# Kernel optimization log

Measured on AMD Instinct MI355X. Metric: run time of the kernel, lower is better.

Reference implementation:

```python
import jax, jax.numpy as jnp
import numpy as np

D = 64
NU = 30000
NI = 20000
LU = 50  # mailbox length at user nodes (item_max_length)
LI = 50  # mailbox length at item nodes (user_max_length)


def setup_inputs() -> dict:
    key = jax.random.key(0)
    ks = jax.random.split(key, 14)
    s = 0.05
    return {
        "user_feat": jax.random.normal(ks[0], (NU, D), jnp.float32),
        "item_feat": jax.random.normal(ks[1], (NI, D), jnp.float32),
        "W_u": jax.random.normal(ks[2], (D, D), jnp.float32) * s,
        "W_i": jax.random.normal(ks[3], (D, D), jnp.float32) * s,
        "Wg_u": jax.random.normal(ks[4], (2 * D, D), jnp.float32) * s,
        "Wg_i": jax.random.normal(ks[5], (2 * D, D), jnp.float32) * s,
        "i_te": jax.random.normal(ks[6], (LI, D), jnp.float32) * s,
        "i_te_k": jax.random.normal(ks[7], (LI, D), jnp.float32) * s,
        "u_te": jax.random.normal(ks[8], (LU, D), jnp.float32) * s,
        "u_te_k": jax.random.normal(ks[9], (LU, D), jnp.float32) * s,
        "item_nbr": jax.random.randint(ks[10], (NI, LI), 0, NU, jnp.int32),
        "item_time": jax.random.randint(ks[11], (NI, LI), 0, 1000000, jnp.int32),
        "user_nbr": jax.random.randint(ks[12], (NU, LU), 0, NI, jnp.int32),
        "user_time": jax.random.randint(ks[13], (NU, LU), 0, 1000000, jnp.int32),
    }


def _orgat_att(src_mb, dst_h, time, te, te_k):
    """One DGSR reduce: long-term time-encoded attention + short-term last-attention.
    src_mb: [N, L, d] gathered source features; dst_h: [N, d]; time: [N, L] int.
    Returns concat([h_long, h_short]) @ Wg applied by caller.
    """
    L = time.shape[1]
    d = src_mb.shape[-1]
    scale = jnp.sqrt(jnp.asarray(d, src_mb.dtype))
    # rank of each edge's time within the neighborhood; re_order: 0 = most recent
    rank = jnp.argsort(jnp.argsort(time, axis=1), axis=1)
    re_o = L - rank - 1                                       # [N, L]
    e = jnp.sum((te[re_o] + src_mb) * dst_h[:, None, :], axis=2) / scale
    alpha = jax.nn.softmax(e, axis=1)                         # [N, L]
    h_long = jnp.sum(alpha[..., None] * (src_mb + te_k[re_o]), axis=1)
    # short-term: attention keyed on the most-recent neighbor
    last = jnp.argmax(time, axis=1)
    last_em = jnp.take_along_axis(src_mb, last[:, None, None], axis=1)  # [N,1,d]
    e1 = jnp.sum(last_em * src_mb, axis=2) / scale
    a1 = jax.nn.softmax(e1, axis=1)
    h_short = jnp.sum(a1[..., None] * src_mb, axis=1)
    return jnp.concatenate([h_long, h_short], axis=-1)        # [N, 2d]


def reference(user_feat, item_feat, W_u, W_i, Wg_u, Wg_i, i_te, i_te_k,
              u_te, u_te_k, item_nbr, item_time, user_nbr, user_time):
    uh = user_feat @ W_u   # user_weight (feat_drop=0)
    ih = item_feat @ W_i   # item_weight
    # 'by' edges: users -> items (item reduce uses user mailboxes + i_time_encoding)
    u_mb = uh[item_nbr]                                        # [NI, LI, d]
    item_new = _orgat_att(u_mb, ih, item_time, i_te, i_te_k) @ Wg_i
    # 'pby' edges: items -> users (user reduce uses item mailboxes + u_time_encoding)
    i_mb = ih[user_nbr]                                        # [NU, LU, d]
    user_new = _orgat_att(i_mb, uh, user_time, u_te, u_te_k) @ Wg_u
    # residual update functions
    user_out = jax.nn.elu(user_new + user_feat)
    item_out = jax.nn.elu(item_new + item_feat)
    return user_out, item_out
```

## Files before the change

### kernel.cpp

```cpp
#include <hip/hip_runtime.h>
#include <stdint.h>

#define D   64
#define L   50
#define NUM_U 30000
#define NUM_I 20000
#define MROWS 50
#define PW3 (MROWS * 32 + 96 + 192)
#define GEMM_BLKS 782


typedef __attribute__((ext_vector_type(8))) short short8x;
typedef __attribute__((ext_vector_type(4))) float f32x4;

__device__ __forceinline__ float lof(unsigned int u) {
    union { unsigned int i; float f; } v; v.i = u << 16; return v.f;
}
__device__ __forceinline__ float hif(unsigned int u) {
    union { unsigned int i; float f; } v; v.i = u & 0xffff0000u; return v.f;
}
__device__ __forceinline__ unsigned int f2bfbits(float f) {
    union { float f; unsigned int i; } v; v.f = f;
    return (v.i + 0x7fffu + ((v.i >> 16) & 1u)) >> 16;
}
__device__ __forceinline__ unsigned int packbf(float a, float b) {
    return f2bfbits(a) | (f2bfbits(b) << 16);
}
__device__ __forceinline__ float rl(float v, int l) {
    return __int_as_float(__builtin_amdgcn_readlane(__float_as_int(v), l));
}
__device__ __forceinline__ int rli(int v, int l) {
    return __builtin_amdgcn_readlane(v, l);
}
__device__ __forceinline__ void gload_lds16(const void* g, void* l) {
    __builtin_amdgcn_global_load_lds(
        (const __attribute__((address_space(1))) unsigned int*)g,
        (__attribute__((address_space(3))) unsigned int*)l, 16, 0, 0);
}

__global__ __launch_bounds__(256) void prep(
    const float* __restrict__ user_feat, const float* __restrict__ item_feat,
    const float* __restrict__ W_u, const float* __restrict__ W_i,
    const float* __restrict__ Wg_i, const float* __restrict__ Wg_u,
    const float* __restrict__ te_i, const float* __restrict__ te_u,
    const float* __restrict__ tk_i, const float* __restrict__ tk_u,
    unsigned int* __restrict__ H,
    unsigned short* __restrict__ WgPi, unsigned short* __restrict__ WgPu,
    unsigned short* __restrict__ tePi, unsigned short* __restrict__ tePu,
    unsigned short* __restrict__ tkPi, unsigned short* __restrict__ tkPu)
{
    const int tid = threadIdx.x;
    if (blockIdx.x < GEMM_BLKS) {
        const int lane = tid & 63, wid = tid >> 6;
        const int tile = blockIdx.x * 4 + wid;
        if (tile >= 3125) return;
        const int r0 = tile * 16;
        const float* src; const float* W;
        if (r0 < NUM_U) { src = user_feat + (size_t)r0 * D;            W = W_u; }
        else            { src = item_feat + (size_t)(r0 - NUM_U) * D;  W = W_i; }
        const int q4 = lane >> 4, c16 = lane & 15;

        short8x bf[2];
#pragma unroll
        for (int kt = 0; kt < 2; kt++) {
            const float* fp = src + c16 * D + kt * 32 + q4 * 8;
            float4 x = *(const float4*)fp;
            float4 y = *(const float4*)(fp + 4);
            union { short8x v; unsigned int u[4]; } t2;
            t2.u[0] = packbf(x.x, x.y); t2.u[1] = packbf(x.z, x.w);
            t2.u[2] = packbf(y.x, y.y); t2.u[3] = packbf(y.z, y.w);
            bf[kt] = t2.v;
        }
        f32x4 zero4 = {0.f, 0.f, 0.f, 0.f};
        f32x4 acc[4];
#pragma unroll
        for (int mt = 0; mt < 4; mt++) acc[mt] = zero4;
#pragma unroll
        for (int kt = 0; kt < 2; kt++) {
#pragma unroll
            for (int mt = 0; mt < 4; mt++) {
                union { short8x v; unsigned short u[8]; } a;
#pragma unroll
                for (int j = 0; j < 8; j++)
                    a.u[j] = (unsigned short)f2bfbits(
                        W[(kt * 32 + q4 * 8 + j) * D + c16 + 16 * mt]);
                acc[mt] = __builtin_amdgcn_mfma_f32_16x16x32_bf16(a.v, bf[kt], acc[mt], 0, 0, 0);
            }
        }
        unsigned int* Hrow = H + (size_t)(r0 + c16) * 32;
#pragma unroll
        for (int mt = 0; mt < 4; mt++) {
            uint2 pk;
            pk.x = packbf(acc[mt][0], acc[mt][1]);
            pk.y = packbf(acc[mt][2], acc[mt][3]);
            *(uint2*)(Hrow + 8 * mt + 2 * q4) = pk;
        }
    } else {
        int gid = (blockIdx.x - GEMM_BLKS) * 256 + tid;
        for (int idx = gid; idx < 8192; idx += 4096) {
            int n = idx >> 7, k = idx & 127;
            WgPi[idx] = (unsigned short)f2bfbits(Wg_i[k * 64 + n]);
            WgPu[idx] = (unsigned short)f2bfbits(Wg_u[k * 64 + n]);
        }
        {
            int idx = gid;
            int r = idx >> 6, k = idx & 63;
            tePi[idx] = (r < L) ? (unsigned short)f2bfbits(te_i[r * 64 + k]) : 0;
            tePu[idx] = (r < L) ? (unsigned short)f2bfbits(te_u[r * 64 + k]) : 0;
            int d = idx >> 6, rr = idx & 63;
            tkPi[idx] = (rr < L) ? (unsigned short)f2bfbits(tk_i[rr * 64 + d]) : 0;
            tkPu[idx] = (rr < L) ? (unsigned short)f2bfbits(tk_u[rr * 64 + d]) : 0;
        }
    }
}

__global__ __launch_bounds__(256, 5) void attn_fused(
    const unsigned int* __restrict__ H,
    const float* __restrict__ user_feat, const float* __restrict__ item_feat,
    const unsigned short* __restrict__ WgPi, const unsigned short* __restrict__ WgPu,
    const unsigned short* __restrict__ tePi, const unsigned short* __restrict__ tePu,
    const unsigned short* __restrict__ tkPi, const unsigned short* __restrict__ tkPu,
    const int* __restrict__ item_nbr, const int* __restrict__ item_time,
    const int* __restrict__ user_nbr, const int* __restrict__ user_time,
    float* __restrict__ out)
{
    __shared__ unsigned int lds[4 * PW3];

    const int tid = threadIdx.x, lane = tid & 63, wid = tid >> 6;
    const bool iside = blockIdx.x < (NUM_I / 4);
    const int bb = iside ? blockIdx.x : blockIdx.x - NUM_I / 4;
    const int n = bb * 4 + wid;
    const int src_base = iside ? 0 : NUM_U;
    const int dst_base = iside ? NUM_U : 0;
    const float* dst_feat = iside ? item_feat : user_feat;
    const unsigned short* WgP  = iside ? WgPi : WgPu;
    const unsigned short* teP  = iside ? tePi : tePu;
    const unsigned short* tekP = iside ? tkPi : tkPu;
    const int* nbr   = iside ? item_nbr  : user_nbr;
    const int* timev = iside ? item_time : user_time;
    float* outp = out + (iside ? (size_t)NUM_U * D : 0);

    const int q4 = lane >> 4, c16 = lane & 15;

    const unsigned int*   Hsrc = H + (size_t)src_base * 32;
    const unsigned short* Hs16 = (const unsigned short*)H + (size_t)src_base * 64;
    const unsigned short* Hd16 = (const unsigned short*)H + (size_t)dst_base * 64;

    unsigned int*   wld  = lds + wid * PW3;
    unsigned int*   mbw  = wld;
    unsigned short* dla  = (unsigned short*)(wld + MROWS * 32);
    float*          escf = (float*)(wld + MROWS * 32 + 96);
    unsigned short* cat  = (unsigned short*)(wld + MROWS * 32 + 96);

    int t   = (lane < L) ? timev[(size_t)n * L + lane] : 0;
    int nbv = (lane < L) ? nbr[(size_t)n * L + lane]  : 0;

    {
        const int soff = (((lane & 7) ^ (lane >> 3)) << 4);
        const int rsel = (lane >> 3) << 2;
#pragma unroll
        for (int g = 0; g < 6; g++) {
            int nb = __builtin_amdgcn_ds_bpermute(rsel + (g << 5), nbv);
            const char* gp = (const char*)(Hsrc + (size_t)(unsigned)nb * 32) + soff;
            gload_lds16(gp, (char*)mbw + (g << 10));
        }
        int row = 48 + (lane >> 5), d = lane & 31;
        int nb = __builtin_amdgcn_ds_bpermute(row << 2, nbv);
        unsigned int v = Hsrc[(size_t)(unsigned)nb * 32 + d];
        mbw[(row << 5) + ((((d >> 2) ^ (row & 7)) << 2) | (d & 3))] = v;
    }

    unsigned int key  = (lane < L) ? ((((unsigned)t) << 6) | (unsigned)lane) : 0u;
    unsigned int key2 = (lane < L) ? ((((unsigned)t) << 6) | (unsigned)(63 - lane)) : 0u;
    int rank = 0;
#pragma unroll
    for (int j = 0; j < L; j++) {
        unsigned int kj = (unsigned int)rli((int)key, j);
        rank += (kj < key) ? 1 : 0;
    }
    int re_o = (lane < L) ? (L - 1 - rank) : lane;

    unsigned int m2 = key2;
#pragma unroll
    for (int s = 32; s; s >>= 1) { unsigned int o2 = __shfl_xor(m2, s); m2 = (o2 > m2) ? o2 : m2; }
    const int last = 63 - (int)(m2 & 63u);

    dla[lane] = Hd16[(size_t)n * 64 + lane];
    int nbl = __shfl(nbv, last);
    dla[64 + lane] = Hs16[(size_t)(unsigned)nbl * 64 + lane];

    f32x4 zero4 = {0.f, 0.f, 0.f, 0.f};
    f32x4 acc_e[4], acc_t[4];
#pragma unroll
    for (int nt = 0; nt < 4; nt++) { acc_e[nt] = zero4; acc_t[nt] = zero4; }
    __builtin_amdgcn_s_setprio(1);
#pragma unroll
    for (int kt = 0; kt < 2; kt++) {
        short8x afr = *(const short8x*)(dla + (c16 & 1) * 64 + kt * 32 + q4 * 8);
        int cc = kt * 4 + q4;
#pragma unroll
        for (int nt = 0; nt < 4; nt++) {
            int row = c16 + 16 * nt;
            int rowc = (row < MROWS) ? row : 0;
            short8x bv = *(const short8x*)((const char*)mbw + rowc * 128
                                           + ((cc ^ (rowc & 7)) << 4));
            acc_e[nt] = __builtin_amdgcn_mfma_f32_16x16x32_bf16(afr, bv, acc_e[nt], 0, 0, 0);
            short8x bt = *(const short8x*)(teP + row * 64 + kt * 32 + q4 * 8);
            acc_t[nt] = __builtin_amdgcn_mfma_f32_16x16x32_bf16(afr, bt, acc_t[nt], 0, 0, 0);
        }
    }
    __builtin_amdgcn_s_setprio(0);
    if (q4 == 0) {
#pragma unroll
        for (int nt = 0; nt < 4; nt++) {
            escf[c16 + 16 * nt]       = acc_e[nt][0];
            escf[64 + c16 + 16 * nt]  = acc_e[nt][1];
            escf[128 + c16 + 16 * nt] = acc_t[nt][0];
        }
    }
    float e  = escf[lane];
    float e1 = escf[64 + lane];
    float th = escf[128 + re_o];

    e = (e + th) * 0.125f;
    e1 *= 0.125f;
    if (lane >= L) { e = -3e38f; e1 = -3e38f; }

    float mx = e;
#pragma unroll
    for (int s = 32; s; s >>= 1) { float o2 = __shfl_xor(mx, s); mx = (o2 > mx) ? o2 : mx; }
    float ex = __expf(e - mx);
    float sm = ex;
#pragma unroll
    for (int s = 32; s; s >>= 1) sm += __shfl_xor(sm, s);
    float alpha = ex / sm;

    float mx1 = e1;
#pragma unroll
    for (int s = 32; s; s >>= 1) { float o2 = __shfl_xor(mx1, s); mx1 = (o2 > mx1) ? o2 : mx1; }
    float ex1 = __expf(e1 - mx1);
    float sm1 = ex1;
#pragma unroll
    for (int s = 32; s; s >>= 1) sm1 += __shfl_xor(sm1, s);
    float aw = ex1 / sm1;

    dla[lane]       = (unsigned short)f2bfbits(alpha);
    dla[64 + lane]  = (unsigned short)f2bfbits(aw);
    dla[128 + re_o] = (unsigned short)f2bfbits(alpha);

    f32x4 acc_s[4], acc_k[4];
#pragma unroll
    for (int nt = 0; nt < 4; nt++) { acc_s[nt] = zero4; acc_k[nt] = zero4; }
    __builtin_amdgcn_s_setprio(1);
#pragma unroll
    for (int kt = 0; kt < 2; kt++) {
        short8x aS = *(const short8x*)(dla + (c16 & 1) * 64 + kt * 32 + q4 * 8);
        short8x aB = *(const short8x*)(dla + 128 + kt * 32 + q4 * 8);
        int kr128[8];
#pragma unroll
        for (int i = 0; i < 8; i++) {
            int k = kt * 32 + q4 * 8 + i;
            if (kt) k = (k < MROWS) ? k : (k - 32);
            kr128[i] = k << 7;
        }
#pragma unroll
        for (int nt = 0; nt < 4; nt++) {
            int dc = c16 + 16 * nt;
            int t3 = dc >> 3;
            const char* cbase = (const char*)mbw + ((dc & 7) << 1);
            union { short8x v; unsigned short u[8]; } bu;
#pragma unroll
            for (int i = 0; i < 8; i++)
                bu.u[i] = *(const unsigned short*)(cbase + kr128[i] + ((t3 ^ i) << 4));
            acc_s[nt] = __builtin_amdgcn_mfma_f32_16x16x32_bf16(aS, bu.v, acc_s[nt], 0, 0, 0);
            short8x bK = *(const short8x*)(tekP + dc * 64 + kt * 32 + q4 * 8);
            acc_k[nt] = __builtin_amdgcn_mfma_f32_16x16x32_bf16(aB, bK, acc_k[nt], 0, 0, 0);
        }
    }
    __builtin_amdgcn_s_setprio(0);
    if (q4 == 0) {
#pragma unroll
        for (int nt = 0; nt < 4; nt++) {
            cat[c16 + 16 * nt]      = (unsigned short)f2bfbits(acc_s[nt][0] + acc_k[nt][0]);
            cat[64 + c16 + 16 * nt] = (unsigned short)f2bfbits(acc_s[nt][1]);
        }
    }
    __syncthreads();

    short8x bfr[4];
#pragma unroll
    for (int tK = 0; tK < 4; tK++)
        bfr[tK] = *(const short8x*)(WgP + (wid * 16 + c16) * 128 + tK * 32 + q4 * 8);

    const unsigned short* catw =
        (const unsigned short*)(lds + (lane & 3) * PW3 + MROWS * 32 + 96);
    f32x4 acc = zero4;
#pragma unroll
    for (int tK = 0; tK < 4; tK++) {
        short8x a = *(const short8x*)(catw + tK * 32 + q4 * 8);
        acc = __builtin_amdgcn_mfma_f32_16x16x32_bf16(a, bfr[tK], acc, 0, 0, 0);
    }
    float r01 = (q4 & 1) ? acc[1] : acc[0];
    float r23 = (q4 & 1) ? acc[3] : acc[2];
    float pv  = (q4 & 2) ? r23 : r01;

    int node = bb * 4 + q4;
    float fres = dst_feat[(size_t)node * D + wid * 16 + c16];
    float oo = pv + fres;
    oo = (oo > 0.f) ? oo : (__expf(oo) - 1.f);
    outp[(size_t)node * D + wid * 16 + c16] = oo;
}

__global__ __launch_bounds__(256) void attn_mono(
    const float* __restrict__ src_feat, const float* __restrict__ dst_feat,
    const float* __restrict__ W_src, const float* __restrict__ W_dst,
    const float* __restrict__ Wg, const float* __restrict__ te,
    const float* __restrict__ tek, const int* __restrict__ nbr,
    const int* __restrict__ timev, float* __restrict__ out)
{
    __shared__ unsigned int ws32[64 * 33];
    __shared__ unsigned int te32[L * 33];
    __shared__ unsigned int mbs[4][L * 33];
    const int tid = threadIdx.x, lane = tid & 63, wid = tid >> 6;
    const int n = blockIdx.x * 4 + wid;
    {
        const float2* Wf2 = (const float2*)W_src;
        const float2* Te2 = (const float2*)te;
        for (int idx = tid; idx < 2048; idx += 256) {
            float2 w = Wf2[idx];
            ws32[(idx >> 5) * 33 + (idx & 31)] = packbf(w.x, w.y);
            if (idx < 1600) {
                float2 t2 = Te2[idx];
                te32[(idx >> 5) * 33 + (idx & 31)] = packbf(t2.x, t2.y);
            }
        }
    }
    __syncthreads();
    int t  = (lane < L) ? timev[(size_t)n * L + lane] : 0;
    int nb = (lane < L) ? nbr[(size_t)n * L + lane]  : 0;
    unsigned int key  = (lane < L) ? ((((unsigned)t) << 6) | (unsigned)lane) : 0u;
    unsigned int key2 = (lane < L) ? ((((unsigned)t) << 6) | (unsigned)(63 - lane)) : 0u;
    int rank = 0;
#pragma unroll
    for (int j = 0; j < L; j++) {
        unsigned int kj = (unsigned int)rli((int)key, j);
        rank += (kj < key) ? 1 : 0;
    }
    int re_o = (lane < L) ? (L - 1 - rank) : 0;
    unsigned int m2 = key2;
#pragma unroll
    for (int s = 32; s; s >>= 1) { unsigned int o2 = __shfl_xor(m2, s); m2 = (o2 > m2) ? o2 : m2; }
    const int last = 63 - (int)(m2 & 63u);
    const int rr = (lane < L) ? lane : (L - 1);
    float f = dst_feat[(size_t)n * D + lane];
    float dh;
    {
        float b0 = 0.f, b1 = 0.f, b2 = 0.f, b3 = 0.f;
#pragma unroll
        for (int k = 0; k < 64; k += 4) {
            b0 += rl(f, k + 0) * W_dst[(k + 0) * 64 + lane];
            b1 += rl(f, k + 1) * W_dst[(k + 1) * 64 + lane];
            b2 += rl(f, k + 2) * W_dst[(k + 2) * 64 + lane];
            b3 += rl(f, k + 3) * W_dst[(k + 3) * 64 + lane];
        }
        dh = (b0 + b1) + (b2 + b3);
    }
    float v1;
    {
        float b0 = 0.f, b1 = 0.f, b2 = 0.f, b3 = 0.f;
#pragma unroll
        for (int j = 0; j < 32; j += 2) {
            unsigned int u0 = ws32[lane * 33 + j];
            unsigned int u1 = ws32[lane * 33 + j + 1];
            b0 += lof(u0) * rl(dh, 2 * j + 0);
            b1 += hif(u0) * rl(dh, 2 * j + 1);
            b2 += lof(u1) * rl(dh, 2 * j + 2);
            b3 += hif(u1) * rl(dh, 2 * j + 3);
        }
        v1 = (b0 + b1) + (b2 + b3);
    }
    unsigned int* mbw = mbs[wid];
    {
        const float2* src2 = (const float2*)src_feat;
        int half = lane >> 5, col = lane & 31;
#pragma unroll
        for (int l = 0; l < L; l += 2) {
            int ra = rli(nb, l), rb = rli(nb, l + 1);
            int r = half ? rb : ra;
            float2 v = src2[(size_t)r * 32 + col];
            mbw[(l + half) * 33 + col] = packbf(v.x, v.y);
        }
    }
    __syncthreads();
    unsigned int ul = mbw[last * 33 + (lane >> 1)];
    float rlast = (lane & 1) ? hif(ul) : lof(ul);
    float g;
    {
        float b0 = 0.f, b1 = 0.f, b2 = 0.f, b3 = 0.f;
#pragma unroll
        for (int k = 0; k < 64; k += 4) {
            b0 += rl(rlast, k + 0) * W_src[(k + 0) * 64 + lane];
            b1 += rl(rlast, k + 1) * W_src[(k + 1) * 64 + lane];
            b2 += rl(rlast, k + 2) * W_src[(k + 2) * 64 + lane];
            b3 += rl(rlast, k + 3) * W_src[(k + 3) * 64 + lane];
        }
        g = (b0 + b1) + (b2 + b3);
    }
    float v2;
    {
        float b0 = 0.f, b1 = 0.f, b2 = 0.f, b3 = 0.f;
#pragma unroll
        for (int j = 0; j < 32; j += 2) {
            unsigned int u0 = ws32[lane * 33 + j];
            unsigned int u1 = ws32[lane * 33 + j + 1];
            b0 += lof(u0) * rl(g, 2 * j + 0);
            b1 += hif(u0) * rl(g, 2 * j + 1);
            b2 += lof(u1) * rl(g, 2 * j + 2);
            b3 += hif(u1) * rl(g, 2 * j + 3);
        }
        v2 = (b0 + b1) + (b2 + b3);
    }
    float teh;
    {
        float b0 = 0.f, b1 = 0.f, b2 = 0.f, b3 = 0.f;
#pragma unroll
        for (int j = 0; j < 32; j += 2) {
            unsigned int u0 = te32[rr * 33 + j];
            unsigned int u1 = te32[rr * 33 + j + 1];
            b0 += lof(u0) * rl(dh, 2 * j + 0);
            b1 += hif(u0) * rl(dh, 2 * j + 1);
            b2 += lof(u1) * rl(dh, 2 * j + 2);
            b3 += hif(u1) * rl(dh, 2 * j + 3);
        }
        teh = (b0 + b1) + (b2 + b3);
    }
    float e, e1;
    {
        float ea = 0.f, eb = 0.f, qa = 0.f, qb = 0.f;
#pragma unroll
        for (int j = 0; j < 32; j += 2) {
            unsigned int u0 = mbw[rr * 33 + j];
            unsigned int u1 = mbw[rr * 33 + j + 1];
            float m0 = lof(u0), m1 = hif(u0), m2f = lof(u1), m3 = hif(u1);
            ea += m0 * rl(v1, 2 * j + 0) + m1 * rl(v1, 2 * j + 1);
            eb += m2f * rl(v1, 2 * j + 2) + m3 * rl(v1, 2 * j + 3);
            qa += m0 * rl(v2, 2 * j + 0) + m1 * rl(v2, 2 * j + 1);
            qb += m2f * rl(v2, 2 * j + 2) + m3 * rl(v2, 2 * j + 3);
        }
        e = ea + eb; e1 = qa + qb;
    }
    e = (e + __shfl(teh, re_o)) * 0.125f;
    e1 *= 0.125f;
    if (lane >= L) { e = -3e38f; e1 = -3e38f; }
    float mx = e;
#pragma unroll
    for (int s = 32; s; s >>= 1) { float o2 = __shfl_xor(mx, s); mx = (o2 > mx) ? o2 : mx; }
    float ex = __expf(e - mx);
    float sm = ex;
#pragma unroll
    for (int s = 32; s; s >>= 1) sm += __shfl_xor(sm, s);
    float alpha = ex / sm;
    float mx1 = e1;
#pragma unroll
    for (int s = 32; s; s >>= 1) { float o2 = __shfl_xor(mx1, s); mx1 = (o2 > mx1) ? o2 : mx1; }
    float ex1 = __expf(e1 - mx1);
    float sm1 = ex1;
#pragma unroll
    for (int s = 32; s; s >>= 1) sm1 += __shfl_xor(sm1, s);
    float aw = ex1 / sm1;
    float sl, ss, tacc;
    {
        float sA = 0.f, sB = 0.f, hA = 0.f, hB = 0.f, tA = 0.f, tB = 0.f;
        int hcol = lane >> 1, odd = lane & 1;
#pragma unroll
        for (int l = 0; l < L; l += 2) {
            float saA = rl(alpha, l),     s1A = rl(aw, l);
            float saB = rl(alpha, l + 1), s1B = rl(aw, l + 1);
            int   roA = rli(re_o, l),     roB = rli(re_o, l + 1);
            unsigned int uA = mbw[(l + 0) * 33 + hcol];
            unsigned int uB = mbw[(l + 1) * 33 + hcol];
            float mA = odd ? hif(uA) : lof(uA);
            float mB = odd ? hif(uB) : lof(uB);
            sA += saA * mA; hA += s1A * mA; tA += saA * tek[roA * 64 + lane];
            sB += saB * mB; hB += s1B * mB; tB += saB * tek[roB * 64 + lane];
        }
        sl = sA + sB; ss = hA + hB; tacc = tA + tB;
    }
    float hl, hs;
    {
        float lA = 0.f, lB = 0.f, sA = 0.f, sB = 0.f;
#pragma unroll
        for (int k = 0; k < 64; k += 2) {
            float w0 = W_src[(k + 0) * 64 + lane];
            float w1 = W_src[(k + 1) * 64 + lane];
            lA += rl(sl, k + 0) * w0; sA += rl(ss, k + 0) * w0;
            lB += rl(sl, k + 1) * w1; sB += rl(ss, k + 1) * w1;
        }
        hl = tacc + lA + lB; hs = sA + sB;
    }
    float o;
    {
        float o0 = 0.f, o1 = 0.f, o2 = 0.f, o3 = 0.f;
#pragma unroll
        for (int k = 0; k < 64; k += 2) {
            o0 += rl(hl, k + 0) * Wg[(k + 0) * 64 + lane];
            o1 += rl(hl, k + 1) * Wg[(k + 1) * 64 + lane];
            o2 += rl(hs, k + 0) * Wg[(k + 64) * 64 + lane];
            o3 += rl(hs, k + 1) * Wg[(k + 65) * 64 + lane];
        }
        o = f + (o0 + o1) + (o2 + o3);
    }
    o = (o > 0.f) ? o : (__expf(o) - 1.f);
    out[(size_t)n * D + lane] = o;
}

extern "C" void kernel_launch(void* const* d_in, const int* in_sizes, int n_in,
                              void* d_out, int out_size, void* d_ws, size_t ws_size,
                              hipStream_t stream) {
    const float* user_feat = (const float*)d_in[0];
    const float* item_feat = (const float*)d_in[1];
    const float* W_u  = (const float*)d_in[2];
    const float* W_i  = (const float*)d_in[3];
    const float* Wg_u = (const float*)d_in[4];
    const float* Wg_i = (const float*)d_in[5];
    const float* i_te   = (const float*)d_in[6];
    const float* i_te_k = (const float*)d_in[7];
    const float* u_te   = (const float*)d_in[8];
    const float* u_te_k = (const float*)d_in[9];
    const int* item_nbr  = (const int*)d_in[10];
    const int* item_time = (const int*)d_in[11];
    const int* user_nbr  = (const int*)d_in[12];
    const int* user_time = (const int*)d_in[13];
    (void)in_sizes; (void)n_in; (void)out_size;

    float* outp = (float*)d_out;
    const size_t H_BYTES = (size_t)(NUM_U + NUM_I) * 32 * 4;
    const size_t NEED = H_BYTES + 2 * 16384 + 4 * 8192;

    if (ws_size >= NEED) {
        unsigned int* Hp = (unsigned int*)d_ws;
        unsigned char* aux = (unsigned char*)d_ws + H_BYTES;
        unsigned short* WgPi = (unsigned short*)(aux);
        unsigned short* WgPu = (unsigned short*)(aux + 16384);
        unsigned short* tePi = (unsigned short*)(aux + 32768);
        unsigned short* tePu = (unsigned short*)(aux + 40960);
        unsigned short* tkPi = (unsigned short*)(aux + 49152);
        unsigned short* tkPu = (unsigned short*)(aux + 57344);

        prep<<<GEMM_BLKS + 16, 256, 0, stream>>>(user_feat, item_feat, W_u, W_i,
                                       Wg_i, Wg_u, i_te, u_te, i_te_k, u_te_k,
                                       Hp, WgPi, WgPu, tePi, tePu, tkPi, tkPu);
        attn_fused<<<(NUM_I + NUM_U) / 4, 256, 0, stream>>>(
            Hp, user_feat, item_feat, WgPi, WgPu, tePi, tePu, tkPi, tkPu,
            item_nbr, item_time, user_nbr, user_time, outp);
    } else {
        attn_mono<<<NUM_I / 4, 256, 0, stream>>>(
            user_feat, item_feat, W_u, W_i, Wg_i, i_te, i_te_k,
            item_nbr, item_time, outp + (size_t)NUM_U * D);
        attn_mono<<<NUM_U / 4, 256, 0, stream>>>(
            item_feat, user_feat, W_i, W_u, Wg_u, u_te, u_te_k,
            user_nbr, user_time, outp);
    }
}
```

Baseline: 227.0 us.

## Reswizzle mailbox LDS layout, register-load A fragments, prefetch time-key fragments

Changes the XOR swizzle of the gathered mailbox rows in LDS so it also mixes in row bits 3-4, with the transposed read path adjusted to match. The goal is fewer bank conflicts on both the row-major and column-wise fragment reads. Destination and last-neighbor fragments are now loaded straight from global memory into registers instead of staged through LDS. The te_k B-fragments are prefetched early so their latency overlaps the rank computation. This uses more registers, and the swizzle has to stay consistent between the writes and both read paths.

Result: slower. 252.6 us (+11.3%).

```diff
diff --git a/kernel.cpp b/kernel.cpp
--- a/kernel.cpp
+++ b/kernel.cpp
@@ -161,17 +161,40 @@
 #pragma unroll
         for (int g = 0; g < 6; g++) {
             int nb = __builtin_amdgcn_ds_bpermute(rsel + (g << 5), nbv);
-            const char* gp = (const char*)(Hsrc + (size_t)(unsigned)nb * 32) + soff;
+            const char* gp = (const char*)(Hsrc + (size_t)(unsigned)nb * 32)
+                             + (soff ^ ((g & 3) << 5));
             gload_lds16(gp, (char*)mbw + (g << 10));
         }
         int row = 48 + (lane >> 5), d = lane & 31;
         int nb = __builtin_amdgcn_ds_bpermute(row << 2, nbv);
         unsigned int v = Hsrc[(size_t)(unsigned)nb * 32 + d];
-        mbw[(row << 5) + ((((d >> 2) ^ (row & 7)) << 2) | (d & 3))] = v;
-    }
-
-    unsigned int key  = (lane < L) ? ((((unsigned)t) << 6) | (unsigned)lane) : 0u;
+        int swzr = (row & 7) ^ (((row >> 3) & 3) << 1);
+        mbw[(row << 5) + ((((d >> 2) ^ swzr) << 2) | (d & 3))] = v;
+    }
+
+    short8x bKr[2][4];
+#pragma unroll
+    for (int kt = 0; kt < 2; kt++)
+#pragma unroll
+        for (int nt = 0; nt < 4; nt++)
+            bKr[kt][nt] = *(const short8x*)(tekP + (c16 + 16 * nt) * 64
+                                            + kt * 32 + q4 * 8);
+
     unsigned int key2 = (lane < L) ? ((((unsigned)t) << 6) | (unsigned)(63 - lane)) : 0u;
+    unsigned int m2 = key2;
+#pragma unroll
+    for (int s = 32; s; s >>= 1) { unsigned int o2 = __shfl_xor(m2, s); m2 = (o2 > m2) ? o2 : m2; }
+    const int last = 63 - (int)(m2 & 63u);
+    int nbl = __shfl(nbv, last);
+
+    short8x dhf[2], lmf[2];
+#pragma unroll
+    for (int kt = 0; kt < 2; kt++) {
+        dhf[kt] = *(const short8x*)(Hd16 + (size_t)n * 64 + kt * 32 + q4 * 8);
+        lmf[kt] = *(const short8x*)(Hs16 + (size_t)(unsigned)nbl * 64 + kt * 32 + q4 * 8);
+    }
+
+    unsigned int key = (lane < L) ? ((((unsigned)t) << 6) | (unsigned)lane) : 0u;
     int rank = 0;
 #pragma unroll
     for (int j = 0; j < L; j++) {
@@ -180,15 +203,6 @@
     }
     int re_o = (lane < L) ? (L - 1 - rank) : lane;
 
-    unsigned int m2 = key2;
-#pragma unroll
-    for (int s = 32; s; s >>= 1) { unsigned int o2 = __shfl_xor(m2, s); m2 = (o2 > m2) ? o2 : m2; }
-    const int last = 63 - (int)(m2 & 63u);
-
-    dla[lane] = Hd16[(size_t)n * 64 + lane];
-    int nbl = __shfl(nbv, last);
-    dla[64 + lane] = Hs16[(size_t)(unsigned)nbl * 64 + lane];
-
     f32x4 zero4 = {0.f, 0.f, 0.f, 0.f};
     f32x4 acc_e[4], acc_t[4];
 #pragma unroll
@@ -196,14 +210,15 @@
     __builtin_amdgcn_s_setprio(1);
 #pragma unroll
     for (int kt = 0; kt < 2; kt++) {
-        short8x afr = *(const short8x*)(dla + (c16 & 1) * 64 + kt * 32 + q4 * 8);
+        short8x afr = (c16 & 1) ? lmf[kt] : dhf[kt];
         int cc = kt * 4 + q4;
 #pragma unroll
         for (int nt = 0; nt < 4; nt++) {
             int row = c16 + 16 * nt;
             int rowc = (row < MROWS) ? row : 0;
+            int swzr = (rowc & 7) ^ (((rowc >> 3) & 3) << 1);
             short8x bv = *(const short8x*)((const char*)mbw + rowc * 128
-                                           + ((cc ^ (rowc & 7)) << 4));
+                                           + ((cc ^ swzr) << 4));
             acc_e[nt] = __builtin_amdgcn_mfma_f32_16x16x32_bf16(afr, bv, acc_e[nt], 0, 0, 0);
             short8x bt = *(const short8x*)(teP + row * 64 + kt * 32 + q4 * 8);
             acc_t[nt] = __builtin_amdgcn_mfma_f32_16x16x32_bf16(afr, bt, acc_t[nt], 0, 0, 0);
@@ -263,18 +278,18 @@
             if (kt) k = (k < MROWS) ? k : (k - 32);
             kr128[i] = k << 7;
         }
+        const int qx = q4 << 1;
 #pragma unroll
         for (int nt = 0; nt < 4; nt++) {
             int dc = c16 + 16 * nt;
-            int t3 = dc >> 3;
+            int tq = (dc >> 3) ^ qx;
             const char* cbase = (const char*)mbw + ((dc & 7) << 1);
             union { short8x v; unsigned short u[8]; } bu;
 #pragma unroll
             for (int i = 0; i < 8; i++)
-                bu.u[i] = *(const unsigned short*)(cbase + kr128[i] + ((t3 ^ i) << 4));
+                bu.u[i] = *(const unsigned short*)(cbase + kr128[i] + ((tq ^ i) << 4));
             acc_s[nt] = __builtin_amdgcn_mfma_f32_16x16x32_bf16(aS, bu.v, acc_s[nt], 0, 0, 0);
-            short8x bK = *(const short8x*)(tekP + dc * 64 + kt * 32 + q4 * 8);
-            acc_k[nt] = __builtin_amdgcn_mfma_f32_16x16x32_bf16(aB, bK, acc_k[nt], 0, 0, 0);
+            acc_k[nt] = __builtin_amdgcn_mfma_f32_16x16x32_bf16(aB, bKr[kt][nt], acc_k[nt], 0, 0, 0);
         }
     }
     __builtin_amdgcn_s_setprio(0);
```
